# Performance work log

Measured on AMD Instinct MI355X. Metric: run time of the kernel, lower is better.

The kernel has to match this reference:

```python
import math
import jax, jax.numpy as jnp
import numpy as np

B, S, DM, H = 4, 1024, 1024, 16
D = DM // H


def setup_inputs() -> dict:
    key = jax.random.key(0)
    ks = jax.random.split(key, 8)
    q = jax.random.normal(ks[0], (B, S, DM), dtype=jnp.float32)
    k = jax.random.normal(ks[1], (B, S, DM), dtype=jnp.float32)
    v = jax.random.normal(ks[2], (B, S, DM), dtype=jnp.float32)
    w_scale = 0.02
    Wq = jax.random.normal(ks[3], (DM, DM), dtype=jnp.float32) * w_scale
    Wk = jax.random.normal(ks[4], (DM, DM), dtype=jnp.float32) * w_scale
    Wv = jax.random.normal(ks[5], (DM, DM), dtype=jnp.float32) * w_scale
    Wo = jax.random.normal(ks[6], (DM, DM), dtype=jnp.float32) * w_scale
    bq = jnp.zeros((DM,), jnp.float32)
    bk = jnp.zeros((DM,), jnp.float32)
    bv = jnp.zeros((DM,), jnp.float32)
    bo = jnp.zeros((DM,), jnp.float32)
    # mask==1 means masked (upper triangle above the diagonal)
    causal_mask = jnp.triu(jnp.ones((S, S), jnp.int32), k=1)
    return {"q": q, "k": k, "v": v, "Wq": Wq, "bq": bq, "Wk": Wk, "bk": bk,
            "Wv": Wv, "bv": bv, "Wo": Wo, "bo": bo, "causal_mask": causal_mask}


def reference(q, k, v, Wq, bq, Wk, bk, Wv, bv, Wo, bo, causal_mask):
    Bn, Sq, Dm = q.shape
    # projections (torch Linear: x @ W.T + b)
    qh = (q @ Wq.T + bq).reshape(Bn, Sq, H, D).transpose(0, 2, 1, 3)  # [B,H,S,D]
    kh = (k @ Wk.T + bk).reshape(Bn, -1, H, D).transpose(0, 2, 1, 3)
    vh = (v @ Wv.T + bv).reshape(Bn, -1, H, D).transpose(0, 2, 1, 3)
    # NOTE: module divides by sqrt(d_model), not sqrt(d_head)
    score = jnp.einsum('bhqd,bhkd->bhqk', qh, kh) / math.sqrt(Dm)
    score = jnp.where(causal_mask == 1, jnp.float32(-1e9), score)
    attn_weights = jax.nn.softmax(score, axis=-1)  # dropout is identity in eval
    x = jnp.einsum('bhqk,bhkd->bhqd', attn_weights, vh)
    x = x.transpose(0, 2, 1, 3).reshape(Bn, Sq, Dm)
    x = x @ Wo.T + bo
    present = jnp.stack([kh, vh])  # [2,B,H,S,D]
    return (x, present, attn_weights)
```

## Files before the change

### kernel.cpp

```cpp
#include <hip/hip_runtime.h>


typedef __bf16 bf16x8 __attribute__((ext_vector_type(8)));
typedef float f32x4 __attribute__((ext_vector_type(4)));
typedef unsigned short u16;
typedef unsigned int u32;

#define B_ 4
#define S_ 1024
#define DM_ 1024
#define H_ 16
#define D_ 64

static constexpr size_t N_QKV = (size_t)B_ * S_ * DM_;
static constexpr size_t N_W   = (size_t)DM_ * DM_;

static constexpr size_t QB_OFF = 0;
static constexpr size_t KB_OFF = QB_OFF + N_QKV;
static constexpr size_t VB_OFF = KB_OFF + N_QKV;
static constexpr size_t WQ_OFF = VB_OFF + N_QKV;
static constexpr size_t WK_OFF = WQ_OFF + N_W;
static constexpr size_t WV_OFF = WK_OFF + N_W;
static constexpr size_t WO_OFF = WV_OFF + N_W;
static constexpr size_t QH_OFF = WO_OFF + N_W;
static constexpr size_t KH_OFF = QH_OFF + N_QKV;
static constexpr size_t VT_OFF = KH_OFF + N_QKV;
static constexpr size_t XH_OFF = VT_OFF + N_QKV;

static constexpr size_t P0_OFF = N_QKV;
static constexpr size_t P1_OFF = 2 * N_QKV;
static constexpr size_t AW_OFF = 3 * N_QKV;

__device__ __forceinline__ u16 f2bf(float f) {
    u32 u = __float_as_uint(f);
    u += 0x7FFFu + ((u >> 16) & 1u);
    return (u16)(u >> 16);
}

__device__ __forceinline__ f32x4 zero4() {
    f32x4 z = {0.f, 0.f, 0.f, 0.f};
    return z;
}

__device__ __forceinline__ void async16(const void* g, void* lds) {
    __builtin_amdgcn_global_load_lds(
        (__attribute__((address_space(1))) u32*)g,
        (__attribute__((address_space(3))) u32*)lds,
        16, 0, 0);
}

__global__ __launch_bounds__(256) void cvt_kernel(
    const float* __restrict__ q, const float* __restrict__ k, const float* __restrict__ v,
    const float* __restrict__ wq, const float* __restrict__ wk, const float* __restrict__ wv,
    const float* __restrict__ wo, u16* __restrict__ ws)
{
    const int seg = blockIdx.y;
    const float* src; u16* dst; size_t n;
    switch (seg) {
        case 0: src = q;  dst = ws + QB_OFF; n = N_QKV; break;
        case 1: src = k;  dst = ws + KB_OFF; n = N_QKV; break;
        case 2: src = v;  dst = ws + VB_OFF; n = N_QKV; break;
        case 3: src = wq; dst = ws + WQ_OFF; n = N_W;   break;
        case 4: src = wk; dst = ws + WK_OFF; n = N_W;   break;
        case 5: src = wv; dst = ws + WV_OFF; n = N_W;   break;
        default: src = wo; dst = ws + WO_OFF; n = N_W;  break;
    }
    const size_t idx = ((size_t)blockIdx.x * 256 + threadIdx.x) * 4;
    if (idx >= n) return;
    float4 f = *(const float4*)(src + idx);
    u32 p0 = (u32)f2bf(f.x) | ((u32)f2bf(f.y) << 16);
    u32 p1 = (u32)f2bf(f.z) | ((u32)f2bf(f.w) << 16);
    *(uint2*)(dst + idx) = make_uint2(p0, p1);
}

__device__ __forceinline__ void gemm_mainloop(
    const u16* __restrict__ A, const u16* __restrict__ W, int K,
    int row0, int col0, u16* As, u16* Bs, f32x4 (&acc)[4][4])
{
    const int tid = threadIdx.x;
    const int lane = tid & 63;
    const int w = tid >> 6;
    const int wm = w & 1, wn = w >> 1;
    const int l15 = lane & 15;
    const int acol = (lane >> 4) * 8;

    for (int k0 = 0; k0 < K; k0 += 32) {
#pragma unroll
        for (int j = 0; j < 2; ++j) {
            const int f = (j * 256 + tid) * 16;
            const int r = f >> 6, cb = f & 63;
            async16((const char*)A + ((size_t)(row0 + r) * K + k0) * 2 + cb,
                    (char*)As + j * 4096 + w * 1024);
            async16((const char*)W + ((size_t)(col0 + r) * K + k0) * 2 + cb,
                    (char*)Bs + j * 4096 + w * 1024);
        }
        __syncthreads();
        bf16x8 af[4], bfr[4];
#pragma unroll
        for (int t = 0; t < 4; ++t) {
            af[t]  = *(const bf16x8*)(As + (wm * 64 + t * 16 + l15) * 32 + acol);
            bfr[t] = *(const bf16x8*)(Bs + (wn * 64 + t * 16 + l15) * 32 + acol);
        }
#pragma unroll
        for (int tm = 0; tm < 4; ++tm)
#pragma unroll
            for (int tn = 0; tn < 4; ++tn)
                acc[tm][tn] = __builtin_amdgcn_mfma_f32_16x16x32_bf16(
                    af[tm], bfr[tn], acc[tm][tn], 0, 0, 0);
        __syncthreads();
    }
}

__global__ __launch_bounds__(256) void proj_kernel(
    u16* __restrict__ ws, const float* __restrict__ bq, const float* __restrict__ bk,
    const float* __restrict__ bv, float* __restrict__ out)
{
    const int mode = blockIdx.z;
    const u16* A = ws + QB_OFF + (size_t)mode * N_QKV;
    const u16* W = ws + WQ_OFF + (size_t)mode * N_W;
    const float* bias = (mode == 0) ? bq : (mode == 1 ? bk : bv);
    __shared__ __align__(16) u16 As[128 * 32];
    __shared__ __align__(16) u16 Bs[128 * 32];
    f32x4 acc[4][4];
#pragma unroll
    for (int i = 0; i < 4; ++i)
#pragma unroll
        for (int j = 0; j < 4; ++j) acc[i][j] = zero4();

    const int row0 = blockIdx.x * 128, col0 = blockIdx.y * 128;
    gemm_mainloop(A, W, DM_, row0, col0, As, Bs, acc);

    const int lane = threadIdx.x & 63, w = threadIdx.x >> 6;
    const int wm = w & 1, wn = w >> 1;
    const int quad = lane >> 4, l15 = lane & 15;
#pragma unroll
    for (int tm = 0; tm < 4; ++tm)
#pragma unroll
        for (int tn = 0; tn < 4; ++tn)
#pragma unroll
            for (int i = 0; i < 4; ++i) {
                const int m = row0 + wm * 64 + tm * 16 + quad * 4 + i;
                const int n = col0 + wn * 64 + tn * 16 + l15;
                const float val = acc[tm][tn][i] + bias[n];
                const int b = m >> 10, s = m & (S_ - 1);
                const int h = n >> 6, d = n & 63;
                const size_t hidx = (((size_t)b * H_ + h) * S_ + s) * D_ + d;
                if (mode == 0) {
                    ws[QH_OFF + hidx] = f2bf(val);
                } else if (mode == 1) {
                    out[P0_OFF + hidx] = val;
                    ws[KH_OFF + hidx] = f2bf(val);
                } else {
                    out[P1_OFF + hidx] = val;
                    ws[VT_OFF + (((size_t)b * H_ + h) * D_ + d) * S_ + s] = f2bf(val);
                }
            }
}

__global__ __launch_bounds__(256) void attn_kernel(u16* __restrict__ ws, float* __restrict__ out)
{
    const int qt = blockIdx.x;
    const int h  = blockIdx.y;
    const int b  = blockIdx.z;
    const int bh = b * H_ + h;
    const int q0 = qt * 64;

    const u16* Qg  = ws + QH_OFF + ((size_t)bh * S_ + q0) * D_;
    const u16* Kg  = ws + KH_OFF + (size_t)bh * S_ * D_;
    const u16* Vtg = ws + VT_OFF + (size_t)bh * D_ * S_;
    float* AW = out + AW_OFF + ((size_t)bh * S_ + q0) * S_;
    u16* XH = ws + XH_OFF;

    __shared__ __align__(16) u16 Qs[64 * 64];
    __shared__ __align__(16) u16 Ks[64 * 64];
    __shared__ __align__(16) u16 Vs[64 * 64];
    __shared__ __align__(16) u16 Ps[4][16 * 64];

    const int tid = threadIdx.x;
    const int lane = tid & 63;
    const int w = tid >> 6;
    const int quad = lane >> 4, l15 = lane & 15;

#pragma unroll
    for (int j = 0; j < 2; ++j) {
        const int f = (j * 256 + tid) * 16;
        async16((const char*)Qg + f, (char*)Qs + j * 4096 + w * 1024);
    }

    const int ntiles = qt + 1;
    const float scale = 0.03125f;
    const int qrow = q0 + w * 16 + quad * 4;

    float ps[4] = {0.f, 0.f, 0.f, 0.f};
    for (int t = 0; t < ntiles; ++t) {
        __syncthreads();
#pragma unroll
        for (int j = 0; j < 2; ++j) {
            const int f = (j * 256 + tid) * 16;
            async16((const char*)Kg + (size_t)t * 8192 + f, (char*)Ks + j * 4096 + w * 1024);
        }
        __syncthreads();
        f32x4 sa[4];
        sa[0] = sa[1] = sa[2] = sa[3] = zero4();
#pragma unroll
        for (int kk = 0; kk < 2; ++kk) {
            bf16x8 aq = *(const bf16x8*)(Qs + (w * 16 + l15) * 64 + kk * 32 + quad * 8);
#pragma unroll
            for (int n = 0; n < 4; ++n) {
                bf16x8 bk = *(const bf16x8*)(Ks + (n * 16 + l15) * 64 + kk * 32 + quad * 8);
                sa[n] = __builtin_amdgcn_mfma_f32_16x16x32_bf16(aq, bk, sa[n], 0, 0, 0);
            }
        }
#pragma unroll
        for (int n = 0; n < 4; ++n) {
            const int kcol = t * 64 + n * 16 + l15;
#pragma unroll
            for (int i = 0; i < 4; ++i) {
                float e = (kcol <= qrow + i) ? __expf(sa[n][i] * scale) : 0.f;
                ps[i] += e;
            }
        }
    }

    float rinv[4];
#pragma unroll
    for (int i = 0; i < 4; ++i) {
        float s = ps[i];
        s += __shfl_xor(s, 1);
        s += __shfl_xor(s, 2);
        s += __shfl_xor(s, 4);
        s += __shfl_xor(s, 8);
        rinv[i] = 1.f / s;
    }

    f32x4 oacc[4];
    oacc[0] = oacc[1] = oacc[2] = oacc[3] = zero4();

    for (int t = 0; t < ntiles; ++t) {
        __syncthreads();
#pragma unroll
        for (int j = 0; j < 2; ++j) {
            const int f = (j * 256 + tid) * 16;
            async16((const char*)Kg + (size_t)t * 8192 + f, (char*)Ks + j * 4096 + w * 1024);
            const int d = f >> 7, cb = f & 127;
            async16((const char*)Vtg + (size_t)d * (S_ * 2) + (size_t)t * 128 + cb,
                    (char*)Vs + j * 4096 + w * 1024);
        }
        __syncthreads();
        f32x4 sa[4];
        sa[0] = sa[1] = sa[2] = sa[3] = zero4();
#pragma unroll
        for (int kk = 0; kk < 2; ++kk) {
            bf16x8 aq = *(const bf16x8*)(Qs + (w * 16 + l15) * 64 + kk * 32 + quad * 8);
#pragma unroll
            for (int n = 0; n < 4; ++n) {
                bf16x8 bk = *(const bf16x8*)(Ks + (n * 16 + l15) * 64 + kk * 32 + quad * 8);
                sa[n] = __builtin_amdgcn_mfma_f32_16x16x32_bf16(aq, bk, sa[n], 0, 0, 0);
            }
        }
#pragma unroll
        for (int n = 0; n < 4; ++n) {
            const int kcol = t * 64 + n * 16 + l15;
#pragma unroll
            for (int i = 0; i < 4; ++i) {
                float e = (kcol <= qrow + i) ? __expf(sa[n][i] * scale) : 0.f;
                float wgt = e * rinv[i];
                AW[(size_t)(w * 16 + quad * 4 + i) * S_ + kcol] = wgt;
                Ps[w][(quad * 4 + i) * 64 + n * 16 + l15] = f2bf(wgt);
            }
        }
#pragma unroll
        for (int kk = 0; kk < 2; ++kk) {
            bf16x8 ap = *(const bf16x8*)(&Ps[w][l15 * 64 + kk * 32 + quad * 8]);
#pragma unroll
            for (int n = 0; n < 4; ++n) {
                bf16x8 bv = *(const bf16x8*)(Vs + (n * 16 + l15) * 64 + kk * 32 + quad * 8);
                oacc[n] = __builtin_amdgcn_mfma_f32_16x16x32_bf16(ap, bv, oacc[n], 0, 0, 0);
            }
        }
    }

#pragma unroll
    for (int n = 0; n < 4; ++n)
#pragma unroll
        for (int i = 0; i < 4; ++i) {
            const int qq = q0 + w * 16 + quad * 4 + i;
            const int dc = h * 64 + n * 16 + l15;
            XH[((size_t)b * S_ + qq) * DM_ + dc] = f2bf(oacc[n][i]);
        }

    const int zc0 = ntiles * 64;
    const int Z = S_ - zc0;
    if (Z > 0) {
        const int total = 64 * Z;
        for (int idx = tid * 4; idx < total; idx += 1024) {
            const int r = idx / Z, c = idx - r * Z;
            *(float4*)(&AW[(size_t)r * S_ + zc0 + c]) = make_float4(0.f, 0.f, 0.f, 0.f);
        }
    }
}

__global__ __launch_bounds__(256) void outproj_kernel(
    u16* __restrict__ ws, const float* __restrict__ bo, float* __restrict__ out)
{
    const u16* A = ws + XH_OFF;
    const u16* W = ws + WO_OFF;
    __shared__ __align__(16) u16 As[128 * 32];
    __shared__ __align__(16) u16 Bs[128 * 32];
    f32x4 acc[4][4];
#pragma unroll
    for (int i = 0; i < 4; ++i)
#pragma unroll
        for (int j = 0; j < 4; ++j) acc[i][j] = zero4();

    const int row0 = blockIdx.x * 128, col0 = blockIdx.y * 128;
    gemm_mainloop(A, W, DM_, row0, col0, As, Bs, acc);

    const int lane = threadIdx.x & 63, w = threadIdx.x >> 6;
    const int wm = w & 1, wn = w >> 1;
    const int quad = lane >> 4, l15 = lane & 15;
#pragma unroll
    for (int tm = 0; tm < 4; ++tm)
#pragma unroll
        for (int tn = 0; tn < 4; ++tn)
#pragma unroll
            for (int i = 0; i < 4; ++i) {
                const int m = row0 + wm * 64 + tm * 16 + quad * 4 + i;
                const int n = col0 + wn * 64 + tn * 16 + l15;
                out[(size_t)m * DM_ + n] = acc[tm][tn][i] + bo[n];
            }
}

extern "C" void kernel_launch(void* const* d_in, const int* in_sizes, int n_in,
                              void* d_out, int out_size, void* d_ws, size_t ws_size,
                              hipStream_t stream) {
    const float* q  = (const float*)d_in[0];
    const float* k  = (const float*)d_in[1];
    const float* v  = (const float*)d_in[2];
    const float* Wq = (const float*)d_in[3];
    const float* bq = (const float*)d_in[4];
    const float* Wk = (const float*)d_in[5];
    const float* bk = (const float*)d_in[6];
    const float* Wv = (const float*)d_in[7];
    const float* bv = (const float*)d_in[8];
    const float* Wo = (const float*)d_in[9];
    const float* bo = (const float*)d_in[10];

    u16* ws = (u16*)d_ws;
    float* out = (float*)d_out;
    dim3 blk(256);

    cvt_kernel<<<dim3(4096, 7, 1), blk, 0, stream>>>(q, k, v, Wq, Wk, Wv, Wo, ws);
    proj_kernel<<<dim3(32, 8, 3), blk, 0, stream>>>(ws, bq, bk, bv, out);
    attn_kernel<<<dim3(S_ / 64, H_, B_), blk, 0, stream>>>(ws, out);
    outproj_kernel<<<dim3(32, 8, 1), blk, 0, stream>>>(ws, bo, out);
}
```

Measured before the change: 509.4 us.

## Rework attention to load K/V fragments from global, add V transpose kernel

The attention kernel drops its LDS staging of Q/K/V and the per-tile block barriers; each wave now loads its MFMA fragments straight from global memory. The causal work is scheduled heaviest-first by reversing the query-tile order. V projection output is written in head layout and transposed by a separate LDS-tiled kernel into the freed q-bf16 buffer, replacing the strided scatter store. The cvt launch is flattened into a 1D grid with no idle blocks, and attention-weight stores are moved after the PV MFMAs with a simpler zero-fill. Direct global fragment loads read K/V once per wave instead of once per block and rely on cache, and the extra launch adds overhead.

```diff
diff --git a/kernel.cpp b/kernel.cpp
--- a/kernel.cpp
+++ b/kernel.cpp
@@ -24,8 +24,8 @@
 static constexpr size_t WO_OFF = WV_OFF + N_W;
 static constexpr size_t QH_OFF = WO_OFF + N_W;
 static constexpr size_t KH_OFF = QH_OFF + N_QKV;
-static constexpr size_t VT_OFF = KH_OFF + N_QKV;
-static constexpr size_t XH_OFF = VT_OFF + N_QKV;
+static constexpr size_t VH_OFF = KH_OFF + N_QKV;
+static constexpr size_t XH_OFF = VH_OFF + N_QKV;
 
 static constexpr size_t P0_OFF = N_QKV;
 static constexpr size_t P1_OFF = 2 * N_QKV;
@@ -54,23 +54,24 @@
     const float* __restrict__ wq, const float* __restrict__ wk, const float* __restrict__ wv,
     const float* __restrict__ wo, u16* __restrict__ ws)
 {
-    const int seg = blockIdx.y;
-    const float* src; u16* dst; size_t n;
-    switch (seg) {
-        case 0: src = q;  dst = ws + QB_OFF; n = N_QKV; break;
-        case 1: src = k;  dst = ws + KB_OFF; n = N_QKV; break;
-        case 2: src = v;  dst = ws + VB_OFF; n = N_QKV; break;
-        case 3: src = wq; dst = ws + WQ_OFF; n = N_W;   break;
-        case 4: src = wk; dst = ws + WK_OFF; n = N_W;   break;
-        case 5: src = wv; dst = ws + WV_OFF; n = N_W;   break;
-        default: src = wo; dst = ws + WO_OFF; n = N_W;  break;
-    }
-    const size_t idx = ((size_t)blockIdx.x * 256 + threadIdx.x) * 4;
-    if (idx >= n) return;
-    float4 f = *(const float4*)(src + idx);
+    const size_t e = ((size_t)blockIdx.x * 256 + threadIdx.x) * 4;
+    const float* src; u16* dst;
+    if (e < 3 * N_QKV) {
+        const int seg = (int)(e >> 22);
+        const size_t off = e & (N_QKV - 1);
+        src = (seg == 0 ? q : seg == 1 ? k : v) + off;
+        dst = ws + QB_OFF + (size_t)seg * N_QKV + off;
+    } else {
+        const size_t r = e - 3 * N_QKV;
+        const int seg = (int)(r >> 20);
+        const size_t off = r & (N_W - 1);
+        src = (seg == 0 ? wq : seg == 1 ? wk : seg == 2 ? wv : wo) + off;
+        dst = ws + WQ_OFF + (size_t)seg * N_W + off;
+    }
+    float4 f = *(const float4*)src;
     u32 p0 = (u32)f2bf(f.x) | ((u32)f2bf(f.y) << 16);
     u32 p1 = (u32)f2bf(f.z) | ((u32)f2bf(f.w) << 16);
-    *(uint2*)(dst + idx) = make_uint2(p0, p1);
+    *(uint2*)dst = make_uint2(p0, p1);
 }
 
 __device__ __forceinline__ void gemm_mainloop(
@@ -152,80 +153,96 @@
                     ws[KH_OFF + hidx] = f2bf(val);
                 } else {
                     out[P1_OFF + hidx] = val;
-                    ws[VT_OFF + (((size_t)b * H_ + h) * D_ + d) * S_ + s] = f2bf(val);
+                    ws[VH_OFF + hidx] = f2bf(val);
                 }
             }
 }
 
+__global__ __launch_bounds__(256) void vtrans_kernel(u16* __restrict__ ws)
+{
+    const u16* src = ws + VH_OFF;
+    u16* dst = ws + QB_OFF;
+    const int bh = blockIdx.y;
+    const int s0 = blockIdx.x * 64;
+    __shared__ __align__(16) u16 Ts[64][72];
+    const int tid = threadIdx.x;
+#pragma unroll
+    for (int it = 0; it < 2; ++it) {
+        const int c = it * 256 + tid;
+        const int r = c >> 3, d0 = (c & 7) * 8;
+        bf16x8 vv = *(const bf16x8*)(src + ((size_t)bh * S_ + s0 + r) * D_ + d0);
+        *(bf16x8*)(&Ts[r][d0]) = vv;
+    }
+    __syncthreads();
+#pragma unroll
+    for (int it = 0; it < 2; ++it) {
+        const int c = it * 256 + tid;
+        const int d = c >> 3, sc = (c & 7) * 8;
+        union { u16 u[8]; uint4 v4; } pk;
+#pragma unroll
+        for (int j = 0; j < 8; ++j) pk.u[j] = Ts[sc + j][d];
+        *(uint4*)(dst + ((size_t)bh * D_ + d) * S_ + s0 + sc) = pk.v4;
+    }
+}
+
 __global__ __launch_bounds__(256) void attn_kernel(u16* __restrict__ ws, float* __restrict__ out)
 {
-    const int qt = blockIdx.x;
+    const int qt = (int)gridDim.x - 1 - blockIdx.x;
     const int h  = blockIdx.y;
     const int b  = blockIdx.z;
     const int bh = b * H_ + h;
     const int q0 = qt * 64;
 
-    const u16* Qg  = ws + QH_OFF + ((size_t)bh * S_ + q0) * D_;
-    const u16* Kg  = ws + KH_OFF + (size_t)bh * S_ * D_;
-    const u16* Vtg = ws + VT_OFF + (size_t)bh * D_ * S_;
+    const u16* Qg = ws + QH_OFF + ((size_t)bh * S_ + q0) * D_;
+    const u16* Kg = ws + KH_OFF + (size_t)bh * S_ * D_;
+    const u16* Vt = ws + QB_OFF + (size_t)bh * D_ * S_;
     float* AW = out + AW_OFF + ((size_t)bh * S_ + q0) * S_;
     u16* XH = ws + XH_OFF;
 
-    __shared__ __align__(16) u16 Qs[64 * 64];
-    __shared__ __align__(16) u16 Ks[64 * 64];
-    __shared__ __align__(16) u16 Vs[64 * 64];
-    __shared__ __align__(16) u16 Ps[4][16 * 64];
+    __shared__ __align__(16) u16 Ps[4][16 * 72];
 
     const int tid = threadIdx.x;
     const int lane = tid & 63;
     const int w = tid >> 6;
     const int quad = lane >> 4, l15 = lane & 15;
-
-#pragma unroll
-    for (int j = 0; j < 2; ++j) {
-        const int f = (j * 256 + tid) * 16;
-        async16((const char*)Qg + f, (char*)Qs + j * 4096 + w * 1024);
-    }
+    u16* Pw = &Ps[w][0];
+
+    bf16x8 aq[2];
+    aq[0] = *(const bf16x8*)(Qg + (w * 16 + l15) * 64 + quad * 8);
+    aq[1] = *(const bf16x8*)(Qg + (w * 16 + l15) * 64 + 32 + quad * 8);
 
     const int ntiles = qt + 1;
     const float scale = 0.03125f;
     const int qrow = q0 + w * 16 + quad * 4;
 
-    float ps[4] = {0.f, 0.f, 0.f, 0.f};
+    float ps4[4] = {0.f, 0.f, 0.f, 0.f};
     for (int t = 0; t < ntiles; ++t) {
-        __syncthreads();
-#pragma unroll
-        for (int j = 0; j < 2; ++j) {
-            const int f = (j * 256 + tid) * 16;
-            async16((const char*)Kg + (size_t)t * 8192 + f, (char*)Ks + j * 4096 + w * 1024);
-        }
-        __syncthreads();
+        const u16* Kt = Kg + (size_t)t * 4096;
+        bf16x8 kf[2][4];
+#pragma unroll
+        for (int kk = 0; kk < 2; ++kk)
+#pragma unroll
+            for (int n = 0; n < 4; ++n)
+                kf[kk][n] = *(const bf16x8*)(Kt + (n * 16 + l15) * 64 + kk * 32 + quad * 8);
         f32x4 sa[4];
         sa[0] = sa[1] = sa[2] = sa[3] = zero4();
 #pragma unroll
-        for (int kk = 0; kk < 2; ++kk) {
-            bf16x8 aq = *(const bf16x8*)(Qs + (w * 16 + l15) * 64 + kk * 32 + quad * 8);
-#pragma unroll
-            for (int n = 0; n < 4; ++n) {
-                bf16x8 bk = *(const bf16x8*)(Ks + (n * 16 + l15) * 64 + kk * 32 + quad * 8);
-                sa[n] = __builtin_amdgcn_mfma_f32_16x16x32_bf16(aq, bk, sa[n], 0, 0, 0);
-            }
-        }
+        for (int kk = 0; kk < 2; ++kk)
+#pragma unroll
+            for (int n = 0; n < 4; ++n)
+                sa[n] = __builtin_amdgcn_mfma_f32_16x16x32_bf16(aq[kk], kf[kk][n], sa[n], 0, 0, 0);
 #pragma unroll
         for (int n = 0; n < 4; ++n) {
             const int kcol = t * 64 + n * 16 + l15;
 #pragma unroll
-            for (int i = 0; i < 4; ++i) {
-                float e = (kcol <= qrow + i) ? __expf(sa[n][i] * scale) : 0.f;
-                ps[i] += e;
-            }
-        }
-    }
-
+            for (int i = 0; i < 4; ++i)
+                ps4[i] += (kcol <= qrow + i) ? __expf(sa[n][i] * scale) : 0.f;
+        }
+    }
     float rinv[4];
 #pragma unroll
     for (int i = 0; i < 4; ++i) {
-        float s = ps[i];
+        float s = ps4[i];
         s += __shfl_xor(s, 1);
         s += __shfl_xor(s, 2);
         s += __shfl_xor(s, 4);
@@ -237,46 +254,48 @@
     oacc[0] = oacc[1] = oacc[2] = oacc[3] = zero4();
 
     for (int t = 0; t < ntiles; ++t) {
-        __syncthreads();
-#pragma unroll
-        for (int j = 0; j < 2; ++j) {
-            const int f = (j * 256 + tid) * 16;
-            async16((const char*)Kg + (size_t)t * 8192 + f, (char*)Ks + j * 4096 + w * 1024);
-            const int d = f >> 7, cb = f & 127;
-            async16((const char*)Vtg + (size_t)d * (S_ * 2) + (size_t)t * 128 + cb,
-                    (char*)Vs + j * 4096 + w * 1024);
-        }
-        __syncthreads();
+        const u16* Kt = Kg + (size_t)t * 4096;
+        bf16x8 kf[2][4], vf[2][4];
+#pragma unroll
+        for (int kk = 0; kk < 2; ++kk)
+#pragma unroll
+            for (int n = 0; n < 4; ++n) {
+                kf[kk][n] = *(const bf16x8*)(Kt + (n * 16 + l15) * 64 + kk * 32 + quad * 8);
+                vf[kk][n] = *(const bf16x8*)(Vt + (size_t)(n * 16 + l15) * S_ + t * 64 + kk * 32 + quad * 8);
+            }
         f32x4 sa[4];
         sa[0] = sa[1] = sa[2] = sa[3] = zero4();
 #pragma unroll
-        for (int kk = 0; kk < 2; ++kk) {
-            bf16x8 aq = *(const bf16x8*)(Qs + (w * 16 + l15) * 64 + kk * 32 + quad * 8);
-#pragma unroll
-            for (int n = 0; n < 4; ++n) {
-                bf16x8 bk = *(const bf16x8*)(Ks + (n * 16 + l15) * 64 + kk * 32 + quad * 8);
-                sa[n] = __builtin_amdgcn_mfma_f32_16x16x32_bf16(aq, bk, sa[n], 0, 0, 0);
-            }
-        }
+        for (int kk = 0; kk < 2; ++kk)
+#pragma unroll
+            for (int n = 0; n < 4; ++n)
+                sa[n] = __builtin_amdgcn_mfma_f32_16x16x32_bf16(aq[kk], kf[kk][n], sa[n], 0, 0, 0);
+        float wg[4][4];
 #pragma unroll
         for (int n = 0; n < 4; ++n) {
             const int kcol = t * 64 + n * 16 + l15;
 #pragma unroll
             for (int i = 0; i < 4; ++i) {
-                float e = (kcol <= qrow + i) ? __expf(sa[n][i] * scale) : 0.f;
-                float wgt = e * rinv[i];
-                AW[(size_t)(w * 16 + quad * 4 + i) * S_ + kcol] = wgt;
-                Ps[w][(quad * 4 + i) * 64 + n * 16 + l15] = f2bf(wgt);
+                const float e = (kcol <= qrow + i) ? __expf(sa[n][i] * scale) : 0.f;
+                wg[n][i] = e * rinv[i];
+                Pw[(quad * 4 + i) * 72 + n * 16 + l15] = f2bf(wg[n][i]);
             }
         }
-#pragma unroll
-        for (int kk = 0; kk < 2; ++kk) {
-            bf16x8 ap = *(const bf16x8*)(&Ps[w][l15 * 64 + kk * 32 + quad * 8]);
-#pragma unroll
-            for (int n = 0; n < 4; ++n) {
-                bf16x8 bv = *(const bf16x8*)(Vs + (n * 16 + l15) * 64 + kk * 32 + quad * 8);
-                oacc[n] = __builtin_amdgcn_mfma_f32_16x16x32_bf16(ap, bv, oacc[n], 0, 0, 0);
-            }
+        bf16x8 pa[2];
+#pragma unroll
+        for (int kk = 0; kk < 2; ++kk)
+            pa[kk] = *(const bf16x8*)(Pw + l15 * 72 + kk * 32 + quad * 8);
+#pragma unroll
+        for (int kk = 0; kk < 2; ++kk)
+#pragma unroll
+            for (int n = 0; n < 4; ++n)
+                oacc[n] = __builtin_amdgcn_mfma_f32_16x16x32_bf16(pa[kk], vf[kk][n], oacc[n], 0, 0, 0);
+#pragma unroll
+        for (int n = 0; n < 4; ++n) {
+            const int kcol = t * 64 + n * 16 + l15;
+#pragma unroll
+            for (int i = 0; i < 4; ++i)
+                AW[(size_t)(w * 16 + quad * 4 + i) * S_ + kcol] = wg[n][i];
         }
     }
 
@@ -290,13 +309,12 @@
         }
 
     const int zc0 = ntiles * 64;
-    const int Z = S_ - zc0;
-    if (Z > 0) {
-        const int total = 64 * Z;
-        for (int idx = tid * 4; idx < total; idx += 1024) {
-            const int r = idx / Z, c = idx - r * Z;
-            *(float4*)(&AW[(size_t)r * S_ + zc0 + c]) = make_float4(0.f, 0.f, 0.f, 0.f);
-        }
+    const int Zq = (S_ - zc0) >> 2;
+    if (Zq > 0) {
+        const float4 z4 = make_float4(0.f, 0.f, 0.f, 0.f);
+        for (int r = w; r < 64; r += 4)
+            for (int c = lane; c < Zq; c += 64)
+                *(float4*)(&AW[(size_t)r * S_ + zc0 + c * 4]) = z4;
     }
 }
 
@@ -350,8 +368,9 @@
     float* out = (float*)d_out;
     dim3 blk(256);
 
-    cvt_kernel<<<dim3(4096, 7, 1), blk, 0, stream>>>(q, k, v, Wq, Wk, Wv, Wo, ws);
+    cvt_kernel<<<dim3(16384, 1, 1), blk, 0, stream>>>(q, k, v, Wq, Wk, Wv, Wo, ws);
     proj_kernel<<<dim3(32, 8, 3), blk, 0, stream>>>(ws, bq, bk, bv, out);
+    vtrans_kernel<<<dim3(S_ / 64, B_ * H_, 1), blk, 0, stream>>>(ws);
     attn_kernel<<<dim3(S_ / 64, H_, B_), blk, 0, stream>>>(ws, out);
     outproj_kernel<<<dim3(32, 8, 1), blk, 0, stream>>>(ws, bo, out);
 }
```

Measured after the change: 595.7 us. +16.9%, slower.
